# Kernel tuning notes

Hardware: AMD Instinct MI355X
Metric: run time of the kernel (lower is better)

Reference implementation:

```python
import jax, jax.numpy as jnp
import numpy as np
from jax import lax

A, T, B, OBS, H, ACT = 4, 128, 256, 128, 128, 8  # agents, time, envs, obs_dim, gru_hidden(=embed), act_dim


def setup_inputs() -> dict:
    key = jax.random.key(0)
    ks = jax.random.split(key, 16)
    def w(k, shape, fan_in):
        return (jax.random.normal(k, shape, jnp.float32) / np.float32(np.sqrt(fan_in)))
    return {
        "hstate": jnp.zeros((A, B, H), jnp.float32),
        "obs": jax.random.normal(ks[0], (A, T, B, OBS), jnp.float32),
        "avail_actions": jnp.ones((A, T, B, ACT), jnp.float32),
        # embedding dense
        "We": w(ks[1], (A, OBS, H), OBS), "be": jnp.zeros((A, H), jnp.float32),
        # GRU: input kernels (r|z|n concat) with bias, hidden kernels (r|z|n), only n-hidden has bias
        "Wi": w(ks[2], (A, H, 3 * H), H), "bi": jnp.zeros((A, 3 * H), jnp.float32),
        "Wh": w(ks[3], (A, H, 3 * H), H), "bhn": jnp.zeros((A, H), jnp.float32),
        # actor head
        "Wa1": w(ks[4], (A, H, H), H), "ba1": jnp.zeros((A, H), jnp.float32),
        "Wa2": 0.01 * w(ks[5], (A, H, ACT), H), "ba2": jnp.zeros((A, ACT), jnp.float32),
        "log_std": jnp.zeros((A, ACT), jnp.float32),
        # critic head
        "Wc1": w(ks[6], (A, H, H), H), "bc1": jnp.zeros((A, H), jnp.float32),
        "Wc2": w(ks[7], (A, H, 1), H), "bc2": jnp.zeros((A, 1), jnp.float32),
        "done": jax.random.bernoulli(ks[8], 0.05, (A, T, B)),
    }


def _agent_forward(h0, obs, done, avail_actions, We, be, Wi, bi, Wh, bhn,
                   Wa1, ba1, Wa2, ba2, log_std, Wc1, bc1, Wc2, bc2):
    # obs: [T,B,OBS], done: [T,B], h0: [B,H]
    act = jnp.tanh  # config['network']['activation'] == 'tanh'
    emb = act(jnp.einsum('tbo,oh->tbh', obs, We) + be)          # [T,B,H]
    xi = jnp.einsum('tbh,hg->tbg', emb, Wi) + bi                # [T,B,3H] precomputed input gates

    def step(h, xs):
        xi_t, d = xs                                            # [B,3H], [B]
        h = jnp.where(d[:, None], 0.0, h)                       # reset on done
        hh = h @ Wh                                             # [B,3H]
        xr, xz, xn = jnp.split(xi_t, 3, axis=-1)
        hr, hz, hn = jnp.split(hh, 3, axis=-1)
        r = jax.nn.sigmoid(xr + hr)
        z = jax.nn.sigmoid(xz + hz)
        n = jnp.tanh(xn + r * (hn + bhn))
        h_new = (1.0 - z) * n + z * h
        return h_new, h_new

    hT, ys = lax.scan(step, h0, (xi, done))                     # ys: [T,B,H]
    a = act(jnp.einsum('tbh,hk->tbk', ys, Wa1) + ba1)
    mean = jnp.einsum('tbh,ha->tba', a, Wa2) + ba2              # [T,B,ACT]
    std = jnp.exp(log_std)                                      # [ACT]
    c = act(jnp.einsum('tbh,hk->tbk', ys, Wc1) + bc1)
    value = (jnp.einsum('tbh,ho->tbo', c, Wc2) + bc2)[..., 0]   # [T,B]
    return hT, mean, std, value


def reference(hstate, obs, avail_actions, We, be, Wi, bi, Wh, bhn,
              Wa1, ba1, Wa2, ba2, log_std, Wc1, bc1, Wc2, bc2, done):
    hT, mean, std, value = jax.vmap(_agent_forward)(
        hstate, obs, done, avail_actions, We, be, Wi, bi, Wh, bhn,
        Wa1, ba1, Wa2, ba2, log_std, Wc1, bc1, Wc2, bc2)
    return hT, mean, std, value
```

## Files before the change

kernel.cpp:

```cpp
#include <hip/hip_runtime.h>

typedef unsigned short u16;
typedef __attribute__((ext_vector_type(8))) short short8;
typedef __attribute__((ext_vector_type(4))) float f32x4;

#define A_ 4
#define T_ 128
#define B_ 256
#define OBS_ 128
#define H_ 128
#define G_ 384
#define ACT_ 8

__device__ __forceinline__ u16 f2b(float x) {
    unsigned int u = __float_as_uint(x);
    u = (u + 0x7fffu + ((u >> 16) & 1u)) >> 16;
    return (u16)u;
}
__device__ __forceinline__ u16 f2bc(float x) {
    return (u16)((__float_as_uint(x) + 0x8000u) >> 16);
}
__device__ __forceinline__ float b2f(u16 h) {
    return __uint_as_float(((unsigned int)h) << 16);
}
__device__ __forceinline__ float fexp2_(float x) { return __builtin_amdgcn_exp2f(x); }
__device__ __forceinline__ float frcp_(float x) { return __builtin_amdgcn_rcpf(x); }
__device__ __forceinline__ float sigmoidf_(float x) {
    return frcp_(1.0f + fexp2_(-1.4426950408889634f * x));
}
__device__ __forceinline__ float tanhf_(float x) {
    return 1.0f - 2.0f * frcp_(1.0f + fexp2_(2.8853900817779268f * x));
}
__device__ __forceinline__ f32x4 mfma16(short8 a, short8 b, f32x4 c) {
    return __builtin_amdgcn_mfma_f32_16x16x32_bf16(a, b, c, 0, 0, 0);
}

__global__ void k_prep(const float* __restrict__ We, const float* __restrict__ Wi,
                       const float* __restrict__ Wh, const float* __restrict__ Wa1,
                       const float* __restrict__ Wc1, const float* __restrict__ Wa2,
                       const float* __restrict__ Wc2, const float* __restrict__ log_std,
                       u16* __restrict__ weT, u16* __restrict__ wiT, u16* __restrict__ whT,
                       u16* __restrict__ wa1T, u16* __restrict__ wc1T, u16* __restrict__ h2T,
                       float* __restrict__ std_out) {
    const int PER_A = 149504;
    int idx = blockIdx.x * 256 + threadIdx.x;
    const int total = 4 * PER_A;
    if (idx < total) {
        int a = idx / PER_A;
        int i = idx % PER_A;
        if (i < 16384) {
            int h = i >> 7, o = i & 127;
            weT[a * 16384 + i] = f2b(We[a * 16384 + o * 128 + h]);
        } else if (i < 16384 + 49152) {
            int j = i - 16384; int g = j >> 7, k = j & 127;
            wiT[a * 49152 + j] = f2b(Wi[a * 49152 + k * 384 + g]);
        } else if (i < 16384 + 2 * 49152) {
            int j = i - 16384 - 49152; int g = j >> 7, k = j & 127;
            whT[a * 49152 + j] = f2b(Wh[a * 49152 + k * 384 + g]);
        } else if (i < 2 * 16384 + 2 * 49152) {
            int j = i - 16384 - 2 * 49152; int h2 = j >> 7, k = j & 127;
            wa1T[a * 16384 + j] = f2b(Wa1[a * 16384 + k * 128 + h2]);
        } else if (i < 3 * 16384 + 2 * 49152) {
            int j = i - 2 * 16384 - 2 * 49152; int h2 = j >> 7, k = j & 127;
            wc1T[a * 16384 + j] = f2b(Wc1[a * 16384 + k * 128 + h2]);
        } else {
            int j = i - 3 * 16384 - 2 * 49152; int row = j >> 7, k = j & 127;
            float v = 0.f;
            if (row < 8) v = Wa2[a * 1024 + k * 8 + row];
            else if (row == 8) v = Wc2[a * 128 + k];
            h2T[a * 2048 + j] = f2b(v);
        }
    } else if (idx < total + 32) {
        int i = idx - total;
        std_out[i] = __expf(log_std[i]);
    }
}

__global__ __launch_bounds__(512) void k_embed_xi(
    const float* __restrict__ obs, const float* __restrict__ be, const float* __restrict__ bi,
    const u16* __restrict__ weT, const u16* __restrict__ wiT, u16* __restrict__ xi_ws) {
    __shared__ __align__(16) u16 obsl[16][136];
    __shared__ __align__(16) u16 elds[16][136];
    const int a = blockIdx.y, t = blockIdx.x;
    const int wid = threadIdx.x >> 6, lane = threadIdx.x & 63;
    const int m = lane & 15, quad = lane >> 4;
    const int srow = threadIdx.x >> 5, schunk = threadIdx.x & 31;

    short8 we[4], wi[3][4];
    {
        const u16* p = weT + a * 16384 + (wid * 16 + m) * 128 + quad * 8;
#pragma unroll
        for (int ks = 0; ks < 4; ++ks) we[ks] = *(const short8*)(p + ks * 32);
#pragma unroll
        for (int g = 0; g < 3; ++g) {
            const u16* q = wiT + a * 49152 + (g * 128 + wid * 16 + m) * 128 + quad * 8;
#pragma unroll
            for (int ks = 0; ks < 4; ++ks) wi[g][ks] = *(const short8*)(q + ks * 32);
        }
    }
    const float bee = be[a * H_ + wid * 16 + m];
    float big[3];
#pragma unroll
    for (int g = 0; g < 3; ++g) big[g] = bi[a * G_ + g * 128 + wid * 16 + m];

    const float* obsrow = obs + ((size_t)(a * T_ + t) * B_ + srow) * OBS_ + schunk * 4;
    float4 pf = *(const float4*)(obsrow);
    ushort4* xi4 = (ushort4*)xi_ws;

    for (int it = 0; it < 16; ++it) {
        ushort4 ob;
        ob.x = f2b(pf.x); ob.y = f2b(pf.y); ob.z = f2b(pf.z); ob.w = f2b(pf.w);
        *(ushort4*)&obsl[srow][schunk * 4] = ob;
        __syncthreads();
        if (it + 1 < 16) pf = *(const float4*)(obsrow + (size_t)(it + 1) * 2048);

        short8 af[4];
#pragma unroll
        for (int ks = 0; ks < 4; ++ks)
            af[ks] = *(const short8*)&obsl[m][ks * 32 + quad * 8];
        f32x4 acc = f32x4{0.f, 0.f, 0.f, 0.f};
#pragma unroll
        for (int ks = 0; ks < 4; ++ks) acc = mfma16(af[ks], we[ks], acc);
#pragma unroll
        for (int r = 0; r < 4; ++r)
            elds[quad * 4 + r][wid * 16 + m] = f2b(tanhf_(acc[r] + bee));
        __syncthreads();

        short8 ef[4];
#pragma unroll
        for (int ks = 0; ks < 4; ++ks)
            ef[ks] = *(const short8*)&elds[m][ks * 32 + quad * 8];
        f32x4 xa[3];
#pragma unroll
        for (int g = 0; g < 3; ++g) xa[g] = f32x4{0.f, 0.f, 0.f, 0.f};
#pragma unroll
        for (int ks = 0; ks < 4; ++ks)
#pragma unroll
            for (int g = 0; g < 3; ++g) xa[g] = mfma16(ef[ks], wi[g][ks], xa[g]);

        const size_t base = ((size_t)(a * 16 + it) * T_ + t) * 1536;
#pragma unroll
        for (int g = 0; g < 3; ++g) {
            ushort4 pk;
            pk.x = f2b(xa[g][0] + big[g]);
            pk.y = f2b(xa[g][1] + big[g]);
            pk.z = f2b(xa[g][2] + big[g]);
            pk.w = f2b(xa[g][3] + big[g]);
            xi4[base + (size_t)(wid * 3 + g) * 64 + lane] = pk;
        }
    }
}

__global__ __launch_bounds__(512) void k_scan(
    const float* __restrict__ hstate, const u16* __restrict__ xi_ws,
    const u16* __restrict__ whT, const float* __restrict__ bhn,
    const int* __restrict__ done, u16* __restrict__ ys_ws, float* __restrict__ hT_out) {
    __shared__ __align__(16) u16 hlds[2][16][136];
    const int a = blockIdx.y, btile = blockIdx.x;
    const int wid = threadIdx.x >> 6, lane = threadIdx.x & 63;
    const int m = lane & 15, quad = lane >> 4;
    const int b0 = btile * 16;
    const int col = 16 * wid + m;

    short8 wh[3][4];
    const u16* whTa = whT + a * 49152;
#pragma unroll
    for (int g = 0; g < 3; ++g) {
        const u16* p = whTa + (g * 128 + col) * 128 + quad * 8;
#pragma unroll
        for (int ks = 0; ks < 4; ++ks) wh[g][ks] = *(const short8*)(p + ks * 32);
    }

    float hm[4]; u16 hb[4];
#pragma unroll
    for (int r = 0; r < 4; ++r) {
        float v = hstate[((size_t)a * B_ + b0 + quad * 4 + r) * H_ + col];
        hm[r] = v; hb[r] = f2b(v);
    }
    const float bh = bhn[a * H_ + col];

    const ushort4* xi4 = (const ushort4*)xi_ws;
    const size_t xibase = ((size_t)(a * 16 + btile) * T_) * 1536 + wid * 192 + lane;
    const int* dbase = done + (size_t)a * T_ * B_ + b0 + quad * 4;

    ushort4 px0 = xi4[xibase], px1 = xi4[xibase + 64], px2 = xi4[xibase + 128];
    int dn0 = dbase[0], dn1 = dbase[1], dn2 = dbase[2], dn3 = dbase[3];

    for (int t = 0; t < T_; ++t) {
        u16 (*hl)[136] = hlds[t & 1];
        int dn[4] = {dn0, dn1, dn2, dn3};
#pragma unroll
        for (int r = 0; r < 4; ++r) {
            if (dn[r]) { hm[r] = 0.f; hb[r] = 0; }
            hl[quad * 4 + r][col] = hb[r];
        }
        __syncthreads();

        float xr[4], xz[4], xn[4];
        xr[0] = b2f(px0.x); xr[1] = b2f(px0.y); xr[2] = b2f(px0.z); xr[3] = b2f(px0.w);
        xz[0] = b2f(px1.x); xz[1] = b2f(px1.y); xz[2] = b2f(px1.z); xz[3] = b2f(px1.w);
        xn[0] = b2f(px2.x); xn[1] = b2f(px2.y); xn[2] = b2f(px2.z); xn[3] = b2f(px2.w);
        if (t + 1 < T_) {
            const size_t nx = xibase + (size_t)(t + 1) * 1536;
            px0 = xi4[nx]; px1 = xi4[nx + 64]; px2 = xi4[nx + 128];
            const int* dp = dbase + (size_t)(t + 1) * B_;
            dn0 = dp[0]; dn1 = dp[1]; dn2 = dp[2]; dn3 = dp[3];
        }

        short8 af[4];
#pragma unroll
        for (int ks = 0; ks < 4; ++ks)
            af[ks] = *(const short8*)&hl[m][ks * 32 + quad * 8];

        f32x4 ar = f32x4{0.f, 0.f, 0.f, 0.f};
        f32x4 az = f32x4{0.f, 0.f, 0.f, 0.f};
        f32x4 an = f32x4{0.f, 0.f, 0.f, 0.f};
#pragma unroll
        for (int ks = 0; ks < 4; ++ks) {
            ar = mfma16(af[ks], wh[0][ks], ar);
            az = mfma16(af[ks], wh[1][ks], az);
            an = mfma16(af[ks], wh[2][ks], an);
        }

#pragma unroll
        for (int r = 0; r < 4; ++r) {
            const float rg = sigmoidf_(xr[r] + ar[r]);
            const float zg = sigmoidf_(xz[r] + az[r]);
            const float ng = tanhf_(fmaf(rg, an[r] + bh, xn[r]));
            const float hn2 = fmaf(zg, hm[r] - ng, ng);
            hm[r] = hn2;
            hb[r] = f2bc(hn2);
            ys_ws[(((size_t)a * T_ + t) * B_ + b0 + quad * 4 + r) * H_ + col] = hb[r];
        }
    }
#pragma unroll
    for (int r = 0; r < 4; ++r)
        hT_out[((size_t)a * B_ + b0 + quad * 4 + r) * H_ + col] = hm[r];
}

__global__ __launch_bounds__(512) void k_heads(
    const u16* __restrict__ ys_ws, const u16* __restrict__ wa1T, const u16* __restrict__ wc1T,
    const u16* __restrict__ h2T, const float* __restrict__ ba1, const float* __restrict__ bc1,
    const float* __restrict__ ba2, const float* __restrict__ bc2,
    float* __restrict__ mean_out, float* __restrict__ val_out) {
    __shared__ __align__(16) u16 ysl[16][136];
    __shared__ __align__(16) u16 al[2][16][136];
    const int a = blockIdx.y;
    const int wid = threadIdx.x >> 6, lane = threadIdx.x & 63;
    const int m = lane & 15, quad = lane >> 4;
    const int srow = threadIdx.x >> 5, schunk = threadIdx.x & 31;

    short8 wa[4], wc[4], h2f[4];
    {
        const u16* pa = wa1T + a * 16384 + (wid * 16 + m) * 128 + quad * 8;
        const u16* pc = wc1T + a * 16384 + (wid * 16 + m) * 128 + quad * 8;
        const u16* ph = h2T + a * 2048 + m * 128 + quad * 8;
#pragma unroll
        for (int ks = 0; ks < 4; ++ks) {
            wa[ks] = *(const short8*)(pa + ks * 32);
            wc[ks] = *(const short8*)(pc + ks * 32);
            h2f[ks] = *(const short8*)(ph + ks * 32);
        }
    }
    const float fa = ba1[a * 128 + wid * 16 + m];
    const float fc = bc1[a * 128 + wid * 16 + m];

    const u16* ysbase = ys_ws + ((size_t)a * 32768 + (size_t)blockIdx.x * 256 + srow) * 128 + schunk * 4;
    ushort4 pf = *(const ushort4*)(ysbase);

    for (int it = 0; it < 16; ++it) {
        *(ushort4*)&ysl[srow][schunk * 4] = pf;
        __syncthreads();
        if (it + 1 < 16) pf = *(const ushort4*)(ysbase + (size_t)(it + 1) * 2048);

        short8 yf[4];
#pragma unroll
        for (int ks = 0; ks < 4; ++ks)
            yf[ks] = *(const short8*)&ysl[m][ks * 32 + quad * 8];
        f32x4 aa = f32x4{0.f, 0.f, 0.f, 0.f};
        f32x4 ac = f32x4{0.f, 0.f, 0.f, 0.f};
#pragma unroll
        for (int ks = 0; ks < 4; ++ks) {
            aa = mfma16(yf[ks], wa[ks], aa);
            ac = mfma16(yf[ks], wc[ks], ac);
        }
#pragma unroll
        for (int r = 0; r < 4; ++r) {
            al[0][quad * 4 + r][wid * 16 + m] = f2b(tanhf_(aa[r] + fa));
            al[1][quad * 4 + r][wid * 16 + m] = f2b(tanhf_(ac[r] + fc));
        }
        __syncthreads();

        if (wid < 2) {
            short8 tf[4];
#pragma unroll
            for (int ks = 0; ks < 4; ++ks)
                tf[ks] = *(const short8*)&al[wid][m][ks * 32 + quad * 8];
            f32x4 tacc = f32x4{0.f, 0.f, 0.f, 0.f};
#pragma unroll
            for (int ks = 0; ks < 4; ++ks) tacc = mfma16(tf[ks], h2f[ks], tacc);
            const size_t R0 = (size_t)a * 32768 + (size_t)(blockIdx.x * 16 + it) * 16;
            if (wid == 0) {
                if (m < 8) {
                    const float bb = ba2[a * 8 + m];
#pragma unroll
                    for (int r = 0; r < 4; ++r)
                        mean_out[(R0 + quad * 4 + r) * 8 + m] = tacc[r] + bb;
                }
            } else {
                if (m == 8) {
                    const float bb = bc2[a];
#pragma unroll
                    for (int r = 0; r < 4; ++r)
                        val_out[R0 + quad * 4 + r] = tacc[r] + bb;
                }
            }
        }
    }
}

extern "C" void kernel_launch(void* const* d_in, const int* in_sizes, int n_in,
                              void* d_out, int out_size, void* d_ws, size_t ws_size,
                              hipStream_t stream) {
    const float* hstate = (const float*)d_in[0];
    const float* obs = (const float*)d_in[1];
    const float* We = (const float*)d_in[3];
    const float* be = (const float*)d_in[4];
    const float* Wi = (const float*)d_in[5];
    const float* bi = (const float*)d_in[6];
    const float* Wh = (const float*)d_in[7];
    const float* bhn = (const float*)d_in[8];
    const float* Wa1 = (const float*)d_in[9];
    const float* ba1 = (const float*)d_in[10];
    const float* Wa2 = (const float*)d_in[11];
    const float* ba2 = (const float*)d_in[12];
    const float* log_std = (const float*)d_in[13];
    const float* Wc1 = (const float*)d_in[14];
    const float* bc1 = (const float*)d_in[15];
    const float* Wc2 = (const float*)d_in[16];
    const float* bc2 = (const float*)d_in[17];
    const int* done = (const int*)d_in[18];

    float* out = (float*)d_out;
    float* hT_out = out;
    float* mean_out = out + 131072;
    float* std_out = out + 1179648;
    float* val_out = out + 1179680;

    u16* ws = (u16*)d_ws;
    u16* xi = ws;
    u16* ys = xi + 50331648;
    u16* weT = ys + 16777216;
    u16* wiT = weT + 65536;
    u16* whT = wiT + 196608;
    u16* wa1T = whT + 196608;
    u16* wc1T = wa1T + 65536;
    u16* h2T = wc1T + 65536;

    hipLaunchKernelGGL(k_prep, dim3(2337), dim3(256), 0, stream,
                       We, Wi, Wh, Wa1, Wc1, Wa2, Wc2, log_std,
                       weT, wiT, whT, wa1T, wc1T, h2T, std_out);
    hipLaunchKernelGGL(k_embed_xi, dim3(128, 4), dim3(512), 0, stream,
                       obs, be, bi, weT, wiT, xi);
    hipLaunchKernelGGL(k_scan, dim3(16, 4), dim3(512), 0, stream,
                       hstate, xi, whT, bhn, done, ys, hT_out);
    hipLaunchKernelGGL(k_heads, dim3(128, 4), dim3(512), 0, stream,
                       ys, wa1T, wc1T, h2T, ba1, bc1, ba2, bc2, mean_out, val_out);
}
```

Baseline: 297.3 us.

## Process two batch tiles per scan block and use lighter LDS-only barriers

The GRU scan kernel now gives each block two independent 16-row batch tiles, interleaving their MFMA chains so one tile's latency overlaps the other's work within the serial time loop. Grid size halves to 32 blocks. Input gates are preloaded into the MFMA accumulators, and done flags load as int4. __syncthreads is replaced with a barrier that waits only on LDS counters, and launch_bounds occupancy hints are added. The trade-off is fewer blocks on the GPU and higher register pressure in exchange for more instruction-level parallelism per step. The custom barrier does not wait for outstanding global loads or stores.

```diff
diff --git a/kernel.cpp b/kernel.cpp
--- a/kernel.cpp
+++ b/kernel.cpp
@@ -33,6 +33,9 @@
 }
 __device__ __forceinline__ f32x4 mfma16(short8 a, short8 b, f32x4 c) {
     return __builtin_amdgcn_mfma_f32_16x16x32_bf16(a, b, c, 0, 0, 0);
+}
+__device__ __forceinline__ void barrier_fast() {
+    asm volatile("s_waitcnt lgkmcnt(0)\n\ts_barrier" ::: "memory");
 }
 
 __global__ void k_prep(const float* __restrict__ We, const float* __restrict__ Wi,
@@ -76,7 +79,7 @@
     }
 }
 
-__global__ __launch_bounds__(512) void k_embed_xi(
+__global__ __launch_bounds__(512, 2) void k_embed_xi(
     const float* __restrict__ obs, const float* __restrict__ be, const float* __restrict__ bi,
     const u16* __restrict__ weT, const u16* __restrict__ wiT, u16* __restrict__ xi_ws) {
     __shared__ __align__(16) u16 obsl[16][136];
@@ -111,7 +114,7 @@
         ushort4 ob;
         ob.x = f2b(pf.x); ob.y = f2b(pf.y); ob.z = f2b(pf.z); ob.w = f2b(pf.w);
         *(ushort4*)&obsl[srow][schunk * 4] = ob;
-        __syncthreads();
+        barrier_fast();
         if (it + 1 < 16) pf = *(const float4*)(obsrow + (size_t)(it + 1) * 2048);
 
         short8 af[4];
@@ -124,7 +127,7 @@
 #pragma unroll
         for (int r = 0; r < 4; ++r)
             elds[quad * 4 + r][wid * 16 + m] = f2b(tanhf_(acc[r] + bee));
-        __syncthreads();
+        barrier_fast();
 
         short8 ef[4];
 #pragma unroll
@@ -151,16 +154,15 @@
     }
 }
 
-__global__ __launch_bounds__(512) void k_scan(
+__global__ __launch_bounds__(512, 2) void k_scan(
     const float* __restrict__ hstate, const u16* __restrict__ xi_ws,
     const u16* __restrict__ whT, const float* __restrict__ bhn,
     const int* __restrict__ done, u16* __restrict__ ys_ws, float* __restrict__ hT_out) {
-    __shared__ __align__(16) u16 hlds[2][16][136];
-    const int a = blockIdx.y, btile = blockIdx.x;
-    const int wid = threadIdx.x >> 6, lane = threadIdx.x & 63;
+    __shared__ __align__(16) u16 hlds[2][2][16][136];
+    const int a = blockIdx.y;
+    const int wq = threadIdx.x >> 6, lane = threadIdx.x & 63;
     const int m = lane & 15, quad = lane >> 4;
-    const int b0 = btile * 16;
-    const int col = 16 * wid + m;
+    const int col = 16 * wq + m;
 
     short8 wh[3][4];
     const u16* whTa = whT + a * 49152;
@@ -170,75 +172,110 @@
 #pragma unroll
         for (int ks = 0; ks < 4; ++ks) wh[g][ks] = *(const short8*)(p + ks * 32);
     }
-
-    float hm[4]; u16 hb[4];
+    const float bh = bhn[a * H_ + col];
+
+    const int b00 = blockIdx.x * 32;
+    const int b01 = b00 + 16;
+
+    float hm0[4], hm1[4]; u16 hb0[4], hb1[4];
 #pragma unroll
     for (int r = 0; r < 4; ++r) {
-        float v = hstate[((size_t)a * B_ + b0 + quad * 4 + r) * H_ + col];
-        hm[r] = v; hb[r] = f2b(v);
-    }
-    const float bh = bhn[a * H_ + col];
+        float v0 = hstate[((size_t)a * B_ + b00 + quad * 4 + r) * H_ + col];
+        float v1 = hstate[((size_t)a * B_ + b01 + quad * 4 + r) * H_ + col];
+        hm0[r] = v0; hb0[r] = f2b(v0);
+        hm1[r] = v1; hb1[r] = f2b(v1);
+    }
 
     const ushort4* xi4 = (const ushort4*)xi_ws;
-    const size_t xibase = ((size_t)(a * 16 + btile) * T_) * 1536 + wid * 192 + lane;
-    const int* dbase = done + (size_t)a * T_ * B_ + b0 + quad * 4;
-
-    ushort4 px0 = xi4[xibase], px1 = xi4[xibase + 64], px2 = xi4[xibase + 128];
-    int dn0 = dbase[0], dn1 = dbase[1], dn2 = dbase[2], dn3 = dbase[3];
+    const ushort4* xp0 = xi4 + ((size_t)(a * 16 + blockIdx.x * 2) * T_) * 1536 + wq * 192 + lane;
+    const ushort4* xp1 = xp0 + (size_t)T_ * 1536;
+    const int* dp0 = done + (size_t)a * T_ * B_ + b00 + quad * 4;
+    const int* dp1 = dp0 + 16;
+    u16* yp0 = ys_ws + ((size_t)a * T_ * B_ + b00 + quad * 4) * H_ + col;
+    u16* yp1 = yp0 + 16 * H_;
+
+    ushort4 P00 = xp0[0], P01 = xp0[64], P02 = xp0[128];
+    ushort4 P10 = xp1[0], P11 = xp1[64], P12 = xp1[128];
+    int4 dn0 = *(const int4*)dp0;
+    int4 dn1 = *(const int4*)dp1;
+    xp0 += 1536; xp1 += 1536; dp0 += B_; dp1 += B_;
 
     for (int t = 0; t < T_; ++t) {
-        u16 (*hl)[136] = hlds[t & 1];
-        int dn[4] = {dn0, dn1, dn2, dn3};
+        u16(*hl0)[136] = hlds[0][t & 1];
+        u16(*hl1)[136] = hlds[1][t & 1];
+        if (dn0.x) { hm0[0] = 0.f; hb0[0] = 0; }
+        if (dn0.y) { hm0[1] = 0.f; hb0[1] = 0; }
+        if (dn0.z) { hm0[2] = 0.f; hb0[2] = 0; }
+        if (dn0.w) { hm0[3] = 0.f; hb0[3] = 0; }
+        if (dn1.x) { hm1[0] = 0.f; hb1[0] = 0; }
+        if (dn1.y) { hm1[1] = 0.f; hb1[1] = 0; }
+        if (dn1.z) { hm1[2] = 0.f; hb1[2] = 0; }
+        if (dn1.w) { hm1[3] = 0.f; hb1[3] = 0; }
 #pragma unroll
         for (int r = 0; r < 4; ++r) {
-            if (dn[r]) { hm[r] = 0.f; hb[r] = 0; }
-            hl[quad * 4 + r][col] = hb[r];
-        }
-        __syncthreads();
-
-        float xr[4], xz[4], xn[4];
-        xr[0] = b2f(px0.x); xr[1] = b2f(px0.y); xr[2] = b2f(px0.z); xr[3] = b2f(px0.w);
-        xz[0] = b2f(px1.x); xz[1] = b2f(px1.y); xz[2] = b2f(px1.z); xz[3] = b2f(px1.w);
-        xn[0] = b2f(px2.x); xn[1] = b2f(px2.y); xn[2] = b2f(px2.z); xn[3] = b2f(px2.w);
+            hl0[quad * 4 + r][col] = hb0[r];
+            hl1[quad * 4 + r][col] = hb1[r];
+        }
+        barrier_fast();
+
+        f32x4 ar0, az0, an0, ar1, az1, an1;
+        float xn0[4], xn1[4];
+        ar0[0] = b2f(P00.x); ar0[1] = b2f(P00.y); ar0[2] = b2f(P00.z); ar0[3] = b2f(P00.w);
+        az0[0] = b2f(P01.x); az0[1] = b2f(P01.y); az0[2] = b2f(P01.z); az0[3] = b2f(P01.w);
+        xn0[0] = b2f(P02.x); xn0[1] = b2f(P02.y); xn0[2] = b2f(P02.z); xn0[3] = b2f(P02.w);
+        ar1[0] = b2f(P10.x); ar1[1] = b2f(P10.y); ar1[2] = b2f(P10.z); ar1[3] = b2f(P10.w);
+        az1[0] = b2f(P11.x); az1[1] = b2f(P11.y); az1[2] = b2f(P11.z); az1[3] = b2f(P11.w);
+        xn1[0] = b2f(P12.x); xn1[1] = b2f(P12.y); xn1[2] = b2f(P12.z); xn1[3] = b2f(P12.w);
+        an0 = f32x4{0.f, 0.f, 0.f, 0.f};
+        an1 = f32x4{0.f, 0.f, 0.f, 0.f};
         if (t + 1 < T_) {
-            const size_t nx = xibase + (size_t)(t + 1) * 1536;
-            px0 = xi4[nx]; px1 = xi4[nx + 64]; px2 = xi4[nx + 128];
-            const int* dp = dbase + (size_t)(t + 1) * B_;
-            dn0 = dp[0]; dn1 = dp[1]; dn2 = dp[2]; dn3 = dp[3];
-        }
-
-        short8 af[4];
-#pragma unroll
-        for (int ks = 0; ks < 4; ++ks)
-            af[ks] = *(const short8*)&hl[m][ks * 32 + quad * 8];
-
-        f32x4 ar = f32x4{0.f, 0.f, 0.f, 0.f};
-        f32x4 az = f32x4{0.f, 0.f, 0.f, 0.f};
-        f32x4 an = f32x4{0.f, 0.f, 0.f, 0.f};
+            P00 = xp0[0]; P01 = xp0[64]; P02 = xp0[128]; dn0 = *(const int4*)dp0;
+            P10 = xp1[0]; P11 = xp1[64]; P12 = xp1[128]; dn1 = *(const int4*)dp1;
+        }
+        xp0 += 1536; xp1 += 1536; dp0 += B_; dp1 += B_;
+
+        short8 af0[4], af1[4];
 #pragma unroll
         for (int ks = 0; ks < 4; ++ks) {
-            ar = mfma16(af[ks], wh[0][ks], ar);
-            az = mfma16(af[ks], wh[1][ks], az);
-            an = mfma16(af[ks], wh[2][ks], an);
+            af0[ks] = *(const short8*)&hl0[m][ks * 32 + quad * 8];
+            af1[ks] = *(const short8*)&hl1[m][ks * 32 + quad * 8];
+        }
+#pragma unroll
+        for (int ks = 0; ks < 4; ++ks) {
+            ar0 = mfma16(af0[ks], wh[0][ks], ar0);
+            ar1 = mfma16(af1[ks], wh[0][ks], ar1);
+            az0 = mfma16(af0[ks], wh[1][ks], az0);
+            az1 = mfma16(af1[ks], wh[1][ks], az1);
+            an0 = mfma16(af0[ks], wh[2][ks], an0);
+            an1 = mfma16(af1[ks], wh[2][ks], an1);
         }
 
 #pragma unroll
         for (int r = 0; r < 4; ++r) {
-            const float rg = sigmoidf_(xr[r] + ar[r]);
-            const float zg = sigmoidf_(xz[r] + az[r]);
-            const float ng = tanhf_(fmaf(rg, an[r] + bh, xn[r]));
-            const float hn2 = fmaf(zg, hm[r] - ng, ng);
-            hm[r] = hn2;
-            hb[r] = f2bc(hn2);
-            ys_ws[(((size_t)a * T_ + t) * B_ + b0 + quad * 4 + r) * H_ + col] = hb[r];
-        }
-    }
-#pragma unroll
-    for (int r = 0; r < 4; ++r)
-        hT_out[((size_t)a * B_ + b0 + quad * 4 + r) * H_ + col] = hm[r];
-}
-
-__global__ __launch_bounds__(512) void k_heads(
+            const float rg0 = sigmoidf_(ar0[r]);
+            const float zg0 = sigmoidf_(az0[r]);
+            const float ng0 = tanhf_(fmaf(rg0, an0[r] + bh, xn0[r]));
+            const float h0 = fmaf(zg0, hm0[r] - ng0, ng0);
+            hm0[r] = h0; hb0[r] = f2bc(h0);
+            yp0[(size_t)r * H_] = hb0[r];
+            const float rg1 = sigmoidf_(ar1[r]);
+            const float zg1 = sigmoidf_(az1[r]);
+            const float ng1 = tanhf_(fmaf(rg1, an1[r] + bh, xn1[r]));
+            const float h1 = fmaf(zg1, hm1[r] - ng1, ng1);
+            hm1[r] = h1; hb1[r] = f2bc(h1);
+            yp1[(size_t)r * H_] = hb1[r];
+        }
+        yp0 += (size_t)B_ * H_; yp1 += (size_t)B_ * H_;
+    }
+
+#pragma unroll
+    for (int r = 0; r < 4; ++r) {
+        hT_out[((size_t)a * B_ + b00 + quad * 4 + r) * H_ + col] = hm0[r];
+        hT_out[((size_t)a * B_ + b01 + quad * 4 + r) * H_ + col] = hm1[r];
+    }
+}
+
+__global__ __launch_bounds__(512, 4) void k_heads(
     const u16* __restrict__ ys_ws, const u16* __restrict__ wa1T, const u16* __restrict__ wc1T,
     const u16* __restrict__ h2T, const float* __restrict__ ba1, const float* __restrict__ bc1,
     const float* __restrict__ ba2, const float* __restrict__ bc2,
@@ -270,7 +307,7 @@
 
     for (int it = 0; it < 16; ++it) {
         *(ushort4*)&ysl[srow][schunk * 4] = pf;
-        __syncthreads();
+        barrier_fast();
         if (it + 1 < 16) pf = *(const ushort4*)(ysbase + (size_t)(it + 1) * 2048);
 
         short8 yf[4];
@@ -289,7 +326,7 @@
             al[0][quad * 4 + r][wid * 16 + m] = f2b(tanhf_(aa[r] + fa));
             al[1][quad * 4 + r][wid * 16 + m] = f2b(tanhf_(ac[r] + fc));
         }
-        __syncthreads();
+        barrier_fast();
 
         if (wid < 2) {
             short8 tf[4];
@@ -362,7 +399,7 @@
                        weT, wiT, whT, wa1T, wc1T, h2T, std_out);
     hipLaunchKernelGGL(k_embed_xi, dim3(128, 4), dim3(512), 0, stream,
                        obs, be, bi, weT, wiT, xi);
-    hipLaunchKernelGGL(k_scan, dim3(16, 4), dim3(512), 0, stream,
+    hipLaunchKernelGGL(k_scan, dim3(8, 4), dim3(512), 0, stream,
                        hstate, xi, whT, bhn, done, ys, hT_out);
     hipLaunchKernelGGL(k_heads, dim3(128, 4), dim3(512), 0, stream,
                        ys, wa1T, wc1T, h2T, ba1, bc1, ba2, bc2, mean_out, val_out);
```

Result: slower. 405.9 us (+36.5%).

## Fuse actor/critic heads into the GRU scan kernel, lagging one step

Applied to the files above, without the earlier changes.

Removes the separate heads kernel and the ys workspace round trip. Each scan step now computes the actor and critic heads for the previous timestep's hidden state, reusing the bf16 h tile already staged in LDS, and a tail block handles the last step. It also folds the xi input gates into the MFMA accumulator init and handles done-resets by zeroing the A fragments instead of the LDS values. The cost is extra MFMAs, a second barrier inside the serial recurrence, and higher register pressure from the additional weight fragments, on a grid of only 64 blocks.

```diff
diff --git a/kernel.cpp b/kernel.cpp
--- a/kernel.cpp
+++ b/kernel.cpp
@@ -151,11 +151,16 @@
     }
 }
 
-__global__ __launch_bounds__(512) void k_scan(
+__global__ __launch_bounds__(512, 2) void k_scan(
     const float* __restrict__ hstate, const u16* __restrict__ xi_ws,
     const u16* __restrict__ whT, const float* __restrict__ bhn,
-    const int* __restrict__ done, u16* __restrict__ ys_ws, float* __restrict__ hT_out) {
+    const int* __restrict__ done,
+    const u16* __restrict__ wa1T, const u16* __restrict__ wc1T, const u16* __restrict__ h2T,
+    const float* __restrict__ ba1, const float* __restrict__ bc1,
+    const float* __restrict__ ba2, const float* __restrict__ bc2,
+    float* __restrict__ hT_out, float* __restrict__ mean_out, float* __restrict__ val_out) {
     __shared__ __align__(16) u16 hlds[2][16][136];
+    __shared__ __align__(16) u16 al[2][2][16][136];
     const int a = blockIdx.y, btile = blockIdx.x;
     const int wid = threadIdx.x >> 6, lane = threadIdx.x & 63;
     const int m = lane & 15, quad = lane >> 4;
@@ -170,6 +175,24 @@
 #pragma unroll
         for (int ks = 0; ks < 4; ++ks) wh[g][ks] = *(const short8*)(p + ks * 32);
     }
+    short8 wa[4], wc[4], h2f[4];
+    {
+        const u16* pa = wa1T + a * 16384 + col * 128 + quad * 8;
+        const u16* pc = wc1T + a * 16384 + col * 128 + quad * 8;
+        const u16* ph = h2T + a * 2048 + m * 128 + quad * 8;
+#pragma unroll
+        for (int ks = 0; ks < 4; ++ks) {
+            wa[ks] = *(const short8*)(pa + ks * 32);
+            wc[ks] = *(const short8*)(pc + ks * 32);
+            h2f[ks] = *(const short8*)(ph + ks * 32);
+        }
+    }
+    const float bh = bhn[a * H_ + col];
+    const float fa = ba1[a * 128 + col];
+    const float fc = bc1[a * 128 + col];
+    float bb2 = 0.f;
+    if (wid == 0) { if (m < 8) bb2 = ba2[a * 8 + m]; }
+    else if (wid == 1) { if (m == 8) bb2 = bc2[a]; }
 
     float hm[4]; u16 hb[4];
 #pragma unroll
@@ -177,34 +200,38 @@
         float v = hstate[((size_t)a * B_ + b0 + quad * 4 + r) * H_ + col];
         hm[r] = v; hb[r] = f2b(v);
     }
-    const float bh = bhn[a * H_ + col];
 
     const ushort4* xi4 = (const ushort4*)xi_ws;
     const size_t xibase = ((size_t)(a * 16 + btile) * T_) * 1536 + wid * 192 + lane;
-    const int* dbase = done + (size_t)a * T_ * B_ + b0 + quad * 4;
+    const int* dptr = done + (size_t)a * T_ * B_ + b0 + quad * 4;
+    const int* dAq = done + (size_t)a * T_ * B_ + b0 + m;
 
     ushort4 px0 = xi4[xibase], px1 = xi4[xibase + 64], px2 = xi4[xibase + 128];
-    int dn0 = dbase[0], dn1 = dbase[1], dn2 = dbase[2], dn3 = dbase[3];
+    int4 dn = *(const int4*)(dptr);
+    int dead = dAq[0];
 
     for (int t = 0; t < T_; ++t) {
         u16 (*hl)[136] = hlds[t & 1];
-        int dn[4] = {dn0, dn1, dn2, dn3};
-#pragma unroll
-        for (int r = 0; r < 4; ++r) {
-            if (dn[r]) { hm[r] = 0.f; hb[r] = 0; }
-            hl[quad * 4 + r][col] = hb[r];
-        }
+#pragma unroll
+        for (int r = 0; r < 4; ++r) hl[quad * 4 + r][col] = hb[r];
+        if (dn.x) hm[0] = 0.f;
+        if (dn.y) hm[1] = 0.f;
+        if (dn.z) hm[2] = 0.f;
+        if (dn.w) hm[3] = 0.f;
         __syncthreads();
 
-        float xr[4], xz[4], xn[4];
-        xr[0] = b2f(px0.x); xr[1] = b2f(px0.y); xr[2] = b2f(px0.z); xr[3] = b2f(px0.w);
-        xz[0] = b2f(px1.x); xz[1] = b2f(px1.y); xz[2] = b2f(px1.z); xz[3] = b2f(px1.w);
+        f32x4 ar, az, an;
+        float xn[4];
+        ar[0] = b2f(px0.x); ar[1] = b2f(px0.y); ar[2] = b2f(px0.z); ar[3] = b2f(px0.w);
+        az[0] = b2f(px1.x); az[1] = b2f(px1.y); az[2] = b2f(px1.z); az[3] = b2f(px1.w);
         xn[0] = b2f(px2.x); xn[1] = b2f(px2.y); xn[2] = b2f(px2.z); xn[3] = b2f(px2.w);
+        an = f32x4{0.f, 0.f, 0.f, 0.f};
+        const int deadcur = dead;
         if (t + 1 < T_) {
             const size_t nx = xibase + (size_t)(t + 1) * 1536;
             px0 = xi4[nx]; px1 = xi4[nx + 64]; px2 = xi4[nx + 128];
-            const int* dp = dbase + (size_t)(t + 1) * B_;
-            dn0 = dp[0]; dn1 = dp[1]; dn2 = dp[2]; dn3 = dp[3];
+            dn = *(const int4*)(dptr + (size_t)(t + 1) * B_);
+            dead = dAq[(size_t)(t + 1) * B_];
         }
 
         short8 af[4];
@@ -212,107 +239,118 @@
         for (int ks = 0; ks < 4; ++ks)
             af[ks] = *(const short8*)&hl[m][ks * 32 + quad * 8];
 
-        f32x4 ar = f32x4{0.f, 0.f, 0.f, 0.f};
-        f32x4 az = f32x4{0.f, 0.f, 0.f, 0.f};
-        f32x4 an = f32x4{0.f, 0.f, 0.f, 0.f};
+        f32x4 aa, ac;
+        if (t > 0) {
+            aa = f32x4{fa, fa, fa, fa};
+            ac = f32x4{fc, fc, fc, fc};
+#pragma unroll
+            for (int ks = 0; ks < 4; ++ks) {
+                aa = mfma16(af[ks], wa[ks], aa);
+                ac = mfma16(af[ks], wc[ks], ac);
+            }
+        }
+
+        const short8 z8 = short8{0, 0, 0, 0, 0, 0, 0, 0};
+        short8 afr[4];
+#pragma unroll
+        for (int ks = 0; ks < 4; ++ks) afr[ks] = deadcur ? z8 : af[ks];
 #pragma unroll
         for (int ks = 0; ks < 4; ++ks) {
-            ar = mfma16(af[ks], wh[0][ks], ar);
-            az = mfma16(af[ks], wh[1][ks], az);
-            an = mfma16(af[ks], wh[2][ks], an);
+            ar = mfma16(afr[ks], wh[0][ks], ar);
+            az = mfma16(afr[ks], wh[1][ks], az);
+            an = mfma16(afr[ks], wh[2][ks], an);
+        }
+
+        if (t > 0) {
+#pragma unroll
+            for (int r = 0; r < 4; ++r) {
+                al[t & 1][0][quad * 4 + r][col] = f2b(tanhf_(aa[r]));
+                al[t & 1][1][quad * 4 + r][col] = f2b(tanhf_(ac[r]));
+            }
+            __syncthreads();
         }
 
 #pragma unroll
         for (int r = 0; r < 4; ++r) {
-            const float rg = sigmoidf_(xr[r] + ar[r]);
-            const float zg = sigmoidf_(xz[r] + az[r]);
+            const float rg = sigmoidf_(ar[r]);
+            const float zg = sigmoidf_(az[r]);
             const float ng = tanhf_(fmaf(rg, an[r] + bh, xn[r]));
             const float hn2 = fmaf(zg, hm[r] - ng, ng);
             hm[r] = hn2;
             hb[r] = f2bc(hn2);
-            ys_ws[(((size_t)a * T_ + t) * B_ + b0 + quad * 4 + r) * H_ + col] = hb[r];
-        }
-    }
-#pragma unroll
-    for (int r = 0; r < 4; ++r)
-        hT_out[((size_t)a * B_ + b0 + quad * 4 + r) * H_ + col] = hm[r];
-}
-
-__global__ __launch_bounds__(512) void k_heads(
-    const u16* __restrict__ ys_ws, const u16* __restrict__ wa1T, const u16* __restrict__ wc1T,
-    const u16* __restrict__ h2T, const float* __restrict__ ba1, const float* __restrict__ bc1,
-    const float* __restrict__ ba2, const float* __restrict__ bc2,
-    float* __restrict__ mean_out, float* __restrict__ val_out) {
-    __shared__ __align__(16) u16 ysl[16][136];
-    __shared__ __align__(16) u16 al[2][16][136];
-    const int a = blockIdx.y;
-    const int wid = threadIdx.x >> 6, lane = threadIdx.x & 63;
-    const int m = lane & 15, quad = lane >> 4;
-    const int srow = threadIdx.x >> 5, schunk = threadIdx.x & 31;
-
-    short8 wa[4], wc[4], h2f[4];
-    {
-        const u16* pa = wa1T + a * 16384 + (wid * 16 + m) * 128 + quad * 8;
-        const u16* pc = wc1T + a * 16384 + (wid * 16 + m) * 128 + quad * 8;
-        const u16* ph = h2T + a * 2048 + m * 128 + quad * 8;
-#pragma unroll
-        for (int ks = 0; ks < 4; ++ks) {
-            wa[ks] = *(const short8*)(pa + ks * 32);
-            wc[ks] = *(const short8*)(pc + ks * 32);
-            h2f[ks] = *(const short8*)(ph + ks * 32);
-        }
-    }
-    const float fa = ba1[a * 128 + wid * 16 + m];
-    const float fc = bc1[a * 128 + wid * 16 + m];
-
-    const u16* ysbase = ys_ws + ((size_t)a * 32768 + (size_t)blockIdx.x * 256 + srow) * 128 + schunk * 4;
-    ushort4 pf = *(const ushort4*)(ysbase);
-
-    for (int it = 0; it < 16; ++it) {
-        *(ushort4*)&ysl[srow][schunk * 4] = pf;
-        __syncthreads();
-        if (it + 1 < 16) pf = *(const ushort4*)(ysbase + (size_t)(it + 1) * 2048);
-
-        short8 yf[4];
-#pragma unroll
-        for (int ks = 0; ks < 4; ++ks)
-            yf[ks] = *(const short8*)&ysl[m][ks * 32 + quad * 8];
-        f32x4 aa = f32x4{0.f, 0.f, 0.f, 0.f};
-        f32x4 ac = f32x4{0.f, 0.f, 0.f, 0.f};
-#pragma unroll
-        for (int ks = 0; ks < 4; ++ks) {
-            aa = mfma16(yf[ks], wa[ks], aa);
-            ac = mfma16(yf[ks], wc[ks], ac);
-        }
-#pragma unroll
-        for (int r = 0; r < 4; ++r) {
-            al[0][quad * 4 + r][wid * 16 + m] = f2b(tanhf_(aa[r] + fa));
-            al[1][quad * 4 + r][wid * 16 + m] = f2b(tanhf_(ac[r] + fc));
-        }
-        __syncthreads();
-
-        if (wid < 2) {
+        }
+
+        if (t > 0 && wid < 2) {
             short8 tf[4];
 #pragma unroll
             for (int ks = 0; ks < 4; ++ks)
-                tf[ks] = *(const short8*)&al[wid][m][ks * 32 + quad * 8];
-            f32x4 tacc = f32x4{0.f, 0.f, 0.f, 0.f};
+                tf[ks] = *(const short8*)&al[t & 1][wid][m][ks * 32 + quad * 8];
+            f32x4 tacc = f32x4{bb2, bb2, bb2, bb2};
 #pragma unroll
             for (int ks = 0; ks < 4; ++ks) tacc = mfma16(tf[ks], h2f[ks], tacc);
-            const size_t R0 = (size_t)a * 32768 + (size_t)(blockIdx.x * 16 + it) * 16;
+            const size_t R0 = (size_t)a * 32768 + (size_t)(t - 1) * 256 + b0;
             if (wid == 0) {
                 if (m < 8) {
-                    const float bb = ba2[a * 8 + m];
 #pragma unroll
                     for (int r = 0; r < 4; ++r)
-                        mean_out[(R0 + quad * 4 + r) * 8 + m] = tacc[r] + bb;
+                        mean_out[(R0 + quad * 4 + r) * 8 + m] = tacc[r];
                 }
             } else {
                 if (m == 8) {
-                    const float bb = bc2[a];
 #pragma unroll
                     for (int r = 0; r < 4; ++r)
-                        val_out[R0 + quad * 4 + r] = tacc[r] + bb;
+                        val_out[R0 + quad * 4 + r] = tacc[r];
+                }
+            }
+        }
+    }
+
+#pragma unroll
+    for (int r = 0; r < 4; ++r)
+        hT_out[((size_t)a * B_ + b0 + quad * 4 + r) * H_ + col] = hm[r];
+
+    {
+        u16 (*hl)[136] = hlds[0];
+#pragma unroll
+        for (int r = 0; r < 4; ++r) hl[quad * 4 + r][col] = hb[r];
+        __syncthreads();
+        short8 af[4];
+#pragma unroll
+        for (int ks = 0; ks < 4; ++ks)
+            af[ks] = *(const short8*)&hl[m][ks * 32 + quad * 8];
+        f32x4 aa = f32x4{fa, fa, fa, fa};
+        f32x4 ac = f32x4{fc, fc, fc, fc};
+#pragma unroll
+        for (int ks = 0; ks < 4; ++ks) {
+            aa = mfma16(af[ks], wa[ks], aa);
+            ac = mfma16(af[ks], wc[ks], ac);
+        }
+#pragma unroll
+        for (int r = 0; r < 4; ++r) {
+            al[0][0][quad * 4 + r][col] = f2b(tanhf_(aa[r]));
+            al[0][1][quad * 4 + r][col] = f2b(tanhf_(ac[r]));
+        }
+        __syncthreads();
+        if (wid < 2) {
+            short8 tf[4];
+#pragma unroll
+            for (int ks = 0; ks < 4; ++ks)
+                tf[ks] = *(const short8*)&al[0][wid][m][ks * 32 + quad * 8];
+            f32x4 tacc = f32x4{bb2, bb2, bb2, bb2};
+#pragma unroll
+            for (int ks = 0; ks < 4; ++ks) tacc = mfma16(tf[ks], h2f[ks], tacc);
+            const size_t R0 = (size_t)a * 32768 + (size_t)(T_ - 1) * 256 + b0;
+            if (wid == 0) {
+                if (m < 8) {
+#pragma unroll
+                    for (int r = 0; r < 4; ++r)
+                        mean_out[(R0 + quad * 4 + r) * 8 + m] = tacc[r];
+                }
+            } else {
+                if (m == 8) {
+#pragma unroll
+                    for (int r = 0; r < 4; ++r)
+                        val_out[R0 + quad * 4 + r] = tacc[r];
                 }
             }
         }
@@ -363,7 +401,7 @@
     hipLaunchKernelGGL(k_embed_xi, dim3(128, 4), dim3(512), 0, stream,
                        obs, be, bi, weT, wiT, xi);
     hipLaunchKernelGGL(k_scan, dim3(16, 4), dim3(512), 0, stream,
-                       hstate, xi, whT, bhn, done, ys, hT_out);
-    hipLaunchKernelGGL(k_heads, dim3(128, 4), dim3(512), 0, stream,
-                       ys, wa1T, wc1T, h2T, ba1, bc1, ba2, bc2, mean_out, val_out);
-}
+                       hstate, xi, whT, bhn, done,
+                       wa1T, wc1T, h2T, ba1, bc1, ba2, bc2,
+                       hT_out, mean_out, val_out);
+}
```

Result: slower. 317.7 us (+6.9%).
